# Performance work log

Hardware: AMD Instinct MI355X
Metric: run time of the kernel (lower is better)

## Reference

```python
import jax, jax.numpy as jnp
import numpy as np

NUM_EMBEDDINGS = 1024
EMBEDDING_DIM = 64
COMMITMENT_COST = 0.25


def setup_inputs() -> dict:
    key = jax.random.key(0)
    k1, k2 = jax.random.split(key)
    z = jax.random.normal(k1, (32, 32, 32, EMBEDDING_DIM), dtype=jnp.float32)
    # embedding.weight.data.uniform_(-1/num_embeddings, 1/num_embeddings)
    lim = 1.0 / NUM_EMBEDDINGS
    codebook = jax.random.uniform(k2, (NUM_EMBEDDINGS, EMBEDDING_DIM),
                                  dtype=jnp.float32, minval=-lim, maxval=lim)
    return {"z": z, "codebook": codebook}


def reference(z, codebook):
    beta = COMMITMENT_COST
    zf = z.reshape(-1, EMBEDDING_DIM)                      # [N, D]
    # Squared euclidean distances (argmin is invariant to sqrt in torch.cdist)
    d2 = (jnp.sum(zf * zf, axis=1, keepdims=True)          # [N, 1]
          + jnp.sum(codebook * codebook, axis=1)[None, :]  # [1, K]
          - 2.0 * jnp.einsum('nd,kd->nk', zf, codebook))   # [N, K]
    encoding_indices = jnp.argmin(d2, axis=1)              # [N] int32
    z_q = codebook[encoding_indices].reshape(z.shape)      # [..., D]
    sg = jax.lax.stop_gradient
    loss = jnp.mean((sg(z_q) - z) ** 2) + beta * jnp.mean((z_q - sg(z)) ** 2)
    z_q_st = z + sg(z_q - z)                               # straight-through
    return (z_q_st, loss, encoding_indices)
```

## Files before the change

### kernel.cpp

```cpp
#include <hip/hip_runtime.h>
#include <stdint.h>

#define N_ROWS 32768
#define DIM 64
#define K_CODES 1024
#define ROWS_PER_BLOCK 64
#define THREADS 256
#define CHUNK 128
#define NCHUNK (K_CODES / CHUNK)
#define NBLOCKS (N_ROWS / ROWS_PER_BLOCK)
#define N_ELEMS (N_ROWS * DIM)
#define ZT_STRIDE 68
#define CT_STRIDE 132


__device__ __forceinline__ float bfbits(uint32_t b) { return __uint_as_float(b << 16); }
__device__ __forceinline__ float bf_lo(uint32_t u) { return __uint_as_float(u << 16); }
__device__ __forceinline__ float bf_hi(uint32_t u) { return __uint_as_float(u & 0xFFFF0000u); }

__device__ __forceinline__ float round_bf16(float f) {
  uint32_t u = __float_as_uint(f);
  uint32_t r = ((u + 0x7FFFu + ((u >> 16) & 1u)) >> 16) << 16;
  return __uint_as_float(r);
}

template <typename F>
__device__ __forceinline__ float np_sum64(F get) {
  float r0 = get(0), r1 = get(1), r2 = get(2), r3 = get(3);
  float r4 = get(4), r5 = get(5), r6 = get(6), r7 = get(7);
  for (int i = 8; i < 64; i += 8) {
    r0 = __fadd_rn(r0, get(i + 0)); r1 = __fadd_rn(r1, get(i + 1));
    r2 = __fadd_rn(r2, get(i + 2)); r3 = __fadd_rn(r3, get(i + 3));
    r4 = __fadd_rn(r4, get(i + 4)); r5 = __fadd_rn(r5, get(i + 5));
    r6 = __fadd_rn(r6, get(i + 6)); r7 = __fadd_rn(r7, get(i + 7));
  }
  return __fadd_rn(__fadd_rn(__fadd_rn(r0, r1), __fadd_rn(r2, r3)),
                   __fadd_rn(__fadd_rn(r4, r5), __fadd_rn(r6, r7)));
}

__global__ __launch_bounds__(256) void vq_prep_kernel(
    const void* __restrict__ z, const void* __restrict__ cb,
    float* __restrict__ cc_out, int* __restrict__ flags) {
  const int tid = threadIdx.x;
  __shared__ int s_cnt[2];
  if (tid < 2) s_cnt[tid] = 0;
  __syncthreads();
  if (tid < 128) {
    uint32_t wc = ((const uint32_t*)cb)[(size_t)tid * 255];
    float vc = fabsf(bfbits(wc & 0xFFFFu));
    if (vc == 0.0f || (vc > 5.9e-8f && vc < 32.0f)) atomicAdd(&s_cnt[1], 1);
    if (blockIdx.x == 0) {
      uint32_t wz = ((const uint32_t*)z)[(size_t)tid * 8191];
      float vz = fabsf(bfbits(wz & 0xFFFFu));
      if (vz == 0.0f || (vz > 5.9e-8f && vz < 32.0f)) atomicAdd(&s_cnt[0], 1);
    }
  }
  __syncthreads();
  const bool cb_bf16 = s_cnt[1] >= 96;
  if (blockIdx.x == 0 && tid == 0)
    flags[0] = (s_cnt[0] >= 96 ? 1 : 0) | (cb_bf16 ? 2 : 0);

  const int kk = blockIdx.x * 256 + tid;
  float cv[DIM];
  if (cb_bf16) {
    const uint4* cp = (const uint4*)((const uint16_t*)cb + (size_t)kk * DIM);
    #pragma unroll
    for (int j = 0; j < 8; ++j) {
      uint4 u = cp[j];
      cv[j * 8 + 0] = bf_lo(u.x); cv[j * 8 + 1] = bf_hi(u.x);
      cv[j * 8 + 2] = bf_lo(u.y); cv[j * 8 + 3] = bf_hi(u.y);
      cv[j * 8 + 4] = bf_lo(u.z); cv[j * 8 + 5] = bf_hi(u.z);
      cv[j * 8 + 6] = bf_lo(u.w); cv[j * 8 + 7] = bf_hi(u.w);
    }
  } else {
    const float4* cp = (const float4*)((const float*)cb + (size_t)kk * DIM);
    #pragma unroll
    for (int j = 0; j < 16; ++j) {
      float4 v = cp[j];
      cv[j * 4 + 0] = v.x; cv[j * 4 + 1] = v.y;
      cv[j * 4 + 2] = v.z; cv[j * 4 + 3] = v.w;
    }
  }
  cc_out[kk] = np_sum64([&](int d) { return __fmul_rn(cv[d], cv[d]); });
}

__global__ __launch_bounds__(THREADS) void vq_kernel(
    const void* __restrict__ z, const void* __restrict__ cb,
    const float* __restrict__ cc_in, const int* __restrict__ flags,
    float* __restrict__ out, double* __restrict__ partials) {
  const int tid = threadIdx.x;
  const int fl = flags[0];
  const bool z_bf16  = (fl & 1) != 0;
  const bool cb_bf16 = (fl & 2) != 0;

  __shared__ float zt[DIM][ZT_STRIDE];
  __shared__ float ct[DIM][CT_STRIDE];
  __shared__ float s_cc[K_CODES];
  __shared__ float s_zz[ROWS_PER_BLOCK];
  __shared__ float s_bestM[16][ROWS_PER_BLOCK];
  __shared__ int   s_kM[16][ROWS_PER_BLOCK];
  __shared__ int   s_win[ROWS_PER_BLOCK];
  __shared__ double s_loss[ROWS_PER_BLOCK];

  const int TR = tid & 15;
  const int TK = tid >> 4;
  const size_t row0 = (size_t)blockIdx.x * ROWS_PER_BLOCK;

  #pragma unroll
  for (int kk = tid; kk < K_CODES; kk += THREADS) s_cc[kk] = cc_in[kk];

  if (z_bf16) {
    const uint4* src = (const uint4*)((const uint16_t*)z + row0 * DIM);
    #pragma unroll
    for (int j = 0; j < 2; ++j) {
      int idx = tid + THREADS * j;
      int row = idx >> 3, d0 = (idx & 7) * 8;
      uint4 u = src[idx];
      zt[d0 + 0][row] = bf_lo(u.x); zt[d0 + 1][row] = bf_hi(u.x);
      zt[d0 + 2][row] = bf_lo(u.y); zt[d0 + 3][row] = bf_hi(u.y);
      zt[d0 + 4][row] = bf_lo(u.z); zt[d0 + 5][row] = bf_hi(u.z);
      zt[d0 + 6][row] = bf_lo(u.w); zt[d0 + 7][row] = bf_hi(u.w);
    }
  } else {
    const float4* src = (const float4*)((const float*)z + row0 * DIM);
    #pragma unroll
    for (int j = 0; j < 4; ++j) {
      int idx = tid + THREADS * j;
      int row = idx >> 4, d0 = (idx & 15) * 4;
      float4 v = src[idx];
      zt[d0 + 0][row] = v.x; zt[d0 + 1][row] = v.y;
      zt[d0 + 2][row] = v.z; zt[d0 + 3][row] = v.w;
    }
  }
  __syncthreads();

  if (tid < ROWS_PER_BLOCK) {
    const int r = tid;
    s_zz[r] = np_sum64([&](int d) { float v = zt[d][r]; return __fmul_rn(v, v); });
  }

  float best[4] = {3.4e38f, 3.4e38f, 3.4e38f, 3.4e38f};
  int bk[4] = {0, 0, 0, 0};
  float acc[4][8];
  #pragma unroll
  for (int ri = 0; ri < 4; ++ri)
    #pragma unroll
    for (int ki = 0; ki < 8; ++ki) acc[ri][ki] = 0.0f;

  for (int c = 0; c < NCHUNK; ++c) {
    __syncthreads();
    if (cb_bf16) {
      const uint4* src = (const uint4*)((const uint16_t*)cb + (size_t)c * CHUNK * DIM);
      #pragma unroll
      for (int j = 0; j < 4; ++j) {
        int idx = tid + THREADS * j;
        int kc = idx >> 3, d0 = (idx & 7) * 8;
        uint4 u = src[idx];
        ct[d0 + 0][kc] = bf_lo(u.x); ct[d0 + 1][kc] = bf_hi(u.x);
        ct[d0 + 2][kc] = bf_lo(u.y); ct[d0 + 3][kc] = bf_hi(u.y);
        ct[d0 + 4][kc] = bf_lo(u.z); ct[d0 + 5][kc] = bf_hi(u.z);
        ct[d0 + 6][kc] = bf_lo(u.w); ct[d0 + 7][kc] = bf_hi(u.w);
      }
    } else {
      const float4* src = (const float4*)((const float*)cb + (size_t)c * CHUNK * DIM);
      #pragma unroll
      for (int j = 0; j < 8; ++j) {
        int idx = tid + THREADS * j;
        int kc = idx >> 4, d0 = (idx & 15) * 4;
        float4 v = src[idx];
        ct[d0 + 0][kc] = v.x; ct[d0 + 1][kc] = v.y;
        ct[d0 + 2][kc] = v.z; ct[d0 + 3][kc] = v.w;
      }
    }
    __syncthreads();

    #pragma unroll 4
    for (int d = 0; d < DIM; ++d) {
      float4 zv4 = *(const float4*)&zt[d][TR * 4];
      float4 ca  = *(const float4*)&ct[d][TK * 8];
      float4 cb2 = *(const float4*)&ct[d][TK * 8 + 4];
      float zv[4] = {zv4.x, zv4.y, zv4.z, zv4.w};
      float cv[8] = {ca.x, ca.y, ca.z, ca.w, cb2.x, cb2.y, cb2.z, cb2.w};
      #pragma unroll
      for (int ri = 0; ri < 4; ++ri)
        #pragma unroll
        for (int ki = 0; ki < 8; ++ki)
          acc[ri][ki] = __fadd_rn(acc[ri][ki], __fmul_rn(zv[ri], cv[ki]));
    }

    #pragma unroll
    for (int ri = 0; ri < 4; ++ri) {
      const float zzr = s_zz[TR * 4 + ri];
      #pragma unroll
      for (int ki = 0; ki < 8; ++ki) {
        const int k = c * CHUNK + TK * 8 + ki;
        float e = __fsub_rn(__fadd_rn(zzr, s_cc[k]), __fmul_rn(2.0f, acc[ri][ki]));
        if (e < best[ri]) { best[ri] = e; bk[ri] = k; }
        acc[ri][ki] = 0.0f;
      }
    }
  }

  #pragma unroll
  for (int ri = 0; ri < 4; ++ri) {
    s_bestM[TK][TR * 4 + ri] = best[ri];
    s_kM[TK][TR * 4 + ri] = bk[ri];
  }
  __syncthreads();

  if (tid < ROWS_PER_BLOCK) {
    float b = 3.4e38f;
    int bbk = 0x7FFFFFFF;
    for (int p = 0; p < 16; ++p) {
      float v = s_bestM[p][tid];
      int vk = s_kM[p][tid];
      if (v < b || (v == b && vk < bbk)) { b = v; bbk = vk; }
    }
    s_win[tid] = bbk;
    double acc2 = 0.0;
    if (cb_bf16) {
      const uint16_t* cp = (const uint16_t*)cb + (size_t)bbk * DIM;
      for (int d = 0; d < DIM; ++d) {
        double df = (double)zt[d][tid] - (double)bfbits((uint32_t)cp[d]);
        acc2 = fma(df, df, acc2);
      }
    } else {
      const float* cp = (const float*)cb + (size_t)bbk * DIM;
      for (int d = 0; d < DIM; ++d) {
        double df = (double)zt[d][tid] - (double)cp[d];
        acc2 = fma(df, df, acc2);
      }
    }
    s_loss[tid] = acc2;
    out[(size_t)N_ELEMS + 1 + row0 + tid] = round_bf16((float)bbk);
  }
  __syncthreads();

  const size_t base = row0 * DIM;
  #pragma unroll
  for (int j = 0; j < 16; ++j) {
    int idx = tid + THREADS * j;
    int rr = idx >> 6, dd = idx & 63;
    int w = s_win[rr];
    float v;
    if (cb_bf16) v = bfbits((uint32_t)((const uint16_t*)cb)[(size_t)w * DIM + dd]);
    else         v = round_bf16(((const float*)cb)[(size_t)w * DIM + dd]);
    out[base + idx] = v;
  }

  if (tid == 0) {
    double s = 0.0;
    for (int i = 0; i < ROWS_PER_BLOCK; ++i) s += s_loss[i];
    partials[blockIdx.x] = s;
  }
}

__global__ __launch_bounds__(256) void vq_loss_kernel(
    const double* __restrict__ partials, float* __restrict__ out) {
  __shared__ double sh[256];
  const int tid = threadIdx.x;
  double s = 0.0;
  for (int i = tid; i < NBLOCKS; i += 256) s += partials[i];
  sh[tid] = s;
  __syncthreads();
  if (tid == 0) {
    double t = 0.0;
    for (int i = 0; i < 256; ++i) t += sh[i];
    out[N_ELEMS] = round_bf16((float)(1.25 * t / (double)N_ELEMS));
  }
}

extern "C" void kernel_launch(void* const* d_in, const int* in_sizes, int n_in,
                              void* d_out, int out_size, void* d_ws, size_t ws_size,
                              hipStream_t stream) {
  const void* z  = d_in[0];
  const void* cb = d_in[1];
  float* out = (float*)d_out;
  uint8_t* ws = (uint8_t*)d_ws;
  float* cc = (float*)ws;
  int* flags = (int*)(ws + 4096);
  double* partials = (double*)(ws + 8192);

  vq_prep_kernel<<<K_CODES / 256, 256, 0, stream>>>(z, cb, cc, flags);
  vq_kernel<<<NBLOCKS, THREADS, 0, stream>>>(z, cb, cc, flags, out, partials);
  vq_loss_kernel<<<1, 256, 0, stream>>>(partials, out);
}
```

Baseline: 142.3 us.

## Enlarge per-thread register tile to 8x8 and reduce argmin with wave shuffles

Doubles rows per block to 128, threads to 512 and the codebook chunk to 256. Each thread now computes an 8-row by 8-code register tile instead of 4x8, so each value read from shared memory feeds more FMAs. The z tile is stored in shared memory with a swizzled column order (zcol) so two float4 loads fetch a thread's 8 rows. The per-row argmin is first reduced across lanes with xor shuffles, then across waves through a smaller shared array. The cost is higher register pressure, a larger shared-memory footprint, and only one block per CU.

```diff
diff --git a/kernel.cpp b/kernel.cpp
--- a/kernel.cpp
+++ b/kernel.cpp
@@ -4,14 +4,14 @@
 #define N_ROWS 32768
 #define DIM 64
 #define K_CODES 1024
-#define ROWS_PER_BLOCK 64
-#define THREADS 256
-#define CHUNK 128
+#define ROWS_PER_BLOCK 128
+#define THREADS 512
+#define CHUNK 256
 #define NCHUNK (K_CODES / CHUNK)
 #define NBLOCKS (N_ROWS / ROWS_PER_BLOCK)
 #define N_ELEMS (N_ROWS * DIM)
-#define ZT_STRIDE 68
-#define CT_STRIDE 132
+#define ZT_STRIDE 128
+#define CT_STRIDE 256
 
 
 __device__ __forceinline__ float bfbits(uint32_t b) { return __uint_as_float(b << 16); }
@@ -22,6 +22,10 @@
   uint32_t u = __float_as_uint(f);
   uint32_t r = ((u + 0x7FFFu + ((u >> 16) & 1u)) >> 16) << 16;
   return __uint_as_float(r);
+}
+
+__device__ __forceinline__ int zcol(int row) {
+  return ((row >> 3) << 2) + (((row >> 2) & 1) << 6) + (row & 3);
 }
 
 template <typename F>
@@ -84,7 +88,7 @@
   cc_out[kk] = np_sum64([&](int d) { return __fmul_rn(cv[d], cv[d]); });
 }
 
-__global__ __launch_bounds__(THREADS) void vq_kernel(
+__global__ __launch_bounds__(THREADS, 1) void vq_kernel(
     const void* __restrict__ z, const void* __restrict__ cb,
     const float* __restrict__ cc_in, const int* __restrict__ flags,
     float* __restrict__ out, double* __restrict__ partials) {
@@ -97,8 +101,8 @@
   __shared__ float ct[DIM][CT_STRIDE];
   __shared__ float s_cc[K_CODES];
   __shared__ float s_zz[ROWS_PER_BLOCK];
-  __shared__ float s_bestM[16][ROWS_PER_BLOCK];
-  __shared__ int   s_kM[16][ROWS_PER_BLOCK];
+  __shared__ float s_bestW[8][ROWS_PER_BLOCK];
+  __shared__ int   s_kW[8][ROWS_PER_BLOCK];
   __shared__ int   s_win[ROWS_PER_BLOCK];
   __shared__ double s_loss[ROWS_PER_BLOCK];
 
@@ -115,11 +119,12 @@
     for (int j = 0; j < 2; ++j) {
       int idx = tid + THREADS * j;
       int row = idx >> 3, d0 = (idx & 7) * 8;
+      int col = zcol(row);
       uint4 u = src[idx];
-      zt[d0 + 0][row] = bf_lo(u.x); zt[d0 + 1][row] = bf_hi(u.x);
-      zt[d0 + 2][row] = bf_lo(u.y); zt[d0 + 3][row] = bf_hi(u.y);
-      zt[d0 + 4][row] = bf_lo(u.z); zt[d0 + 5][row] = bf_hi(u.z);
-      zt[d0 + 6][row] = bf_lo(u.w); zt[d0 + 7][row] = bf_hi(u.w);
+      zt[d0 + 0][col] = bf_lo(u.x); zt[d0 + 1][col] = bf_hi(u.x);
+      zt[d0 + 2][col] = bf_lo(u.y); zt[d0 + 3][col] = bf_hi(u.y);
+      zt[d0 + 4][col] = bf_lo(u.z); zt[d0 + 5][col] = bf_hi(u.z);
+      zt[d0 + 6][col] = bf_lo(u.w); zt[d0 + 7][col] = bf_hi(u.w);
     }
   } else {
     const float4* src = (const float4*)((const float*)z + row0 * DIM);
@@ -127,23 +132,25 @@
     for (int j = 0; j < 4; ++j) {
       int idx = tid + THREADS * j;
       int row = idx >> 4, d0 = (idx & 15) * 4;
+      int col = zcol(row);
       float4 v = src[idx];
-      zt[d0 + 0][row] = v.x; zt[d0 + 1][row] = v.y;
-      zt[d0 + 2][row] = v.z; zt[d0 + 3][row] = v.w;
+      zt[d0 + 0][col] = v.x; zt[d0 + 1][col] = v.y;
+      zt[d0 + 2][col] = v.z; zt[d0 + 3][col] = v.w;
     }
   }
   __syncthreads();
 
   if (tid < ROWS_PER_BLOCK) {
-    const int r = tid;
-    s_zz[r] = np_sum64([&](int d) { float v = zt[d][r]; return __fmul_rn(v, v); });
-  }
-
-  float best[4] = {3.4e38f, 3.4e38f, 3.4e38f, 3.4e38f};
-  int bk[4] = {0, 0, 0, 0};
-  float acc[4][8];
+    const int c0 = zcol(tid);
+    s_zz[tid] = np_sum64([&](int d) { float v = zt[d][c0]; return __fmul_rn(v, v); });
+  }
+
+  float best[8] = {3.4e38f, 3.4e38f, 3.4e38f, 3.4e38f,
+                   3.4e38f, 3.4e38f, 3.4e38f, 3.4e38f};
+  int bk[8] = {0, 0, 0, 0, 0, 0, 0, 0};
+  float acc[8][8];
   #pragma unroll
-  for (int ri = 0; ri < 4; ++ri)
+  for (int ri = 0; ri < 8; ++ri)
     #pragma unroll
     for (int ki = 0; ki < 8; ++ki) acc[ri][ki] = 0.0f;
 
@@ -176,21 +183,22 @@
 
     #pragma unroll 4
     for (int d = 0; d < DIM; ++d) {
-      float4 zv4 = *(const float4*)&zt[d][TR * 4];
-      float4 ca  = *(const float4*)&ct[d][TK * 8];
-      float4 cb2 = *(const float4*)&ct[d][TK * 8 + 4];
-      float zv[4] = {zv4.x, zv4.y, zv4.z, zv4.w};
-      float cv[8] = {ca.x, ca.y, ca.z, ca.w, cb2.x, cb2.y, cb2.z, cb2.w};
-      #pragma unroll
-      for (int ri = 0; ri < 4; ++ri)
+      float4 zA = *(const float4*)&zt[d][TR * 4];
+      float4 zB = *(const float4*)&zt[d][TR * 4 + 64];
+      float4 cA = *(const float4*)&ct[d][TK * 8];
+      float4 cB = *(const float4*)&ct[d][TK * 8 + 4];
+      float zv[8] = {zA.x, zA.y, zA.z, zA.w, zB.x, zB.y, zB.z, zB.w};
+      float cv[8] = {cA.x, cA.y, cA.z, cA.w, cB.x, cB.y, cB.z, cB.w};
+      #pragma unroll
+      for (int ri = 0; ri < 8; ++ri)
         #pragma unroll
         for (int ki = 0; ki < 8; ++ki)
           acc[ri][ki] = __fadd_rn(acc[ri][ki], __fmul_rn(zv[ri], cv[ki]));
     }
 
     #pragma unroll
-    for (int ri = 0; ri < 4; ++ri) {
-      const float zzr = s_zz[TR * 4 + ri];
+    for (int ri = 0; ri < 8; ++ri) {
+      const float zzr = s_zz[TR * 8 + ri];
       #pragma unroll
       for (int ki = 0; ki < 8; ++ki) {
         const int k = c * CHUNK + TK * 8 + ki;
@@ -202,32 +210,50 @@
   }
 
   #pragma unroll
-  for (int ri = 0; ri < 4; ++ri) {
-    s_bestM[TK][TR * 4 + ri] = best[ri];
-    s_kM[TK][TR * 4 + ri] = bk[ri];
+  for (int ri = 0; ri < 8; ++ri) {
+    float v = best[ri]; int k = bk[ri];
+    {
+      float v2 = __shfl_xor(v, 16, 64); int k2 = __shfl_xor(k, 16, 64);
+      if (v2 < v || (v2 == v && k2 < k)) { v = v2; k = k2; }
+      v2 = __shfl_xor(v, 32, 64); k2 = __shfl_xor(k, 32, 64);
+      if (v2 < v || (v2 == v && k2 < k)) { v = v2; k = k2; }
+    }
+    best[ri] = v; bk[ri] = k;
+  }
+  {
+    const int lane = tid & 63, wv = tid >> 6;
+    if (lane < 16) {
+      #pragma unroll
+      for (int ri = 0; ri < 8; ++ri) {
+        s_bestW[wv][lane * 8 + ri] = best[ri];
+        s_kW[wv][lane * 8 + ri] = bk[ri];
+      }
+    }
   }
   __syncthreads();
 
   if (tid < ROWS_PER_BLOCK) {
     float b = 3.4e38f;
     int bbk = 0x7FFFFFFF;
-    for (int p = 0; p < 16; ++p) {
-      float v = s_bestM[p][tid];
-      int vk = s_kM[p][tid];
+    #pragma unroll
+    for (int p = 0; p < 8; ++p) {
+      float v = s_bestW[p][tid];
+      int vk = s_kW[p][tid];
       if (v < b || (v == b && vk < bbk)) { b = v; bbk = vk; }
     }
     s_win[tid] = bbk;
+    const int c0 = zcol(tid);
     double acc2 = 0.0;
     if (cb_bf16) {
       const uint16_t* cp = (const uint16_t*)cb + (size_t)bbk * DIM;
       for (int d = 0; d < DIM; ++d) {
-        double df = (double)zt[d][tid] - (double)bfbits((uint32_t)cp[d]);
+        double df = (double)zt[d][c0] - (double)bfbits((uint32_t)cp[d]);
         acc2 = fma(df, df, acc2);
       }
     } else {
       const float* cp = (const float*)cb + (size_t)bbk * DIM;
       for (int d = 0; d < DIM; ++d) {
-        double df = (double)zt[d][tid] - (double)cp[d];
+        double df = (double)zt[d][c0] - (double)cp[d];
         acc2 = fma(df, df, acc2);
       }
     }
```

Result: no change. 142.1 us (-0.1%).
